# Kernel tuning notes

Hardware: AMD Instinct MI355X
Metric: run time of the kernel (lower is better)

Reference implementation:

```python
import jax, jax.numpy as jnp
import numpy as np

K = 5      # neighborhood size (k in torch module)
D_DIL = 4  # dilation (d in torch module)


def _neighbor_indices(H, W, k, d):
    # Matches torch: offsets = range(-(k//2)*d, k*(d//2)+1, d); pairs (i,j) added to (x,y), clamped.
    offs = np.arange(-(k // 2) * d, k * (d // 2) + 1, d)
    pairs = np.array([(i, j) for i in offs for j in offs])  # (k2, 2): i -> x offset, j -> y offset
    y, x = np.meshgrid(np.arange(H), np.arange(W), indexing='ij')
    xi = np.clip(x[None, :, :] + pairs[:, 0, None, None], 0, W - 1)  # (k2, H, W)
    yi = np.clip(y[None, :, :] + pairs[:, 1, None, None], 0, H - 1)  # (k2, H, W)
    return jnp.asarray(yi, jnp.int32), jnp.asarray(xi, jnp.int32)


def _safe_l2(diff):
    # L2 norm over last axis with a grad-safe zero (norm at 0 has subgradient 0, like torch).
    ss = jnp.sum(diff * diff, axis=-1)
    safe = jnp.where(ss > 0, ss, 1.0)
    return jnp.where(ss > 0, jnp.sqrt(safe), 0.0)


def setup_inputs() -> dict:
    key = jax.random.key(0)
    des = jax.random.normal(key, (2, 64, 384, 384), dtype=jnp.float32)
    return {"des": des}


def reference(des):
    B, D, H, W = des.shape
    k2 = K * K
    # per-pixel std of descriptor over channel dim
    mu = jnp.mean(des, axis=1)                                  # (B, H, W)
    s_abs = jnp.sqrt(jnp.mean(des * des, axis=1) - mu * mu)     # (B, H, W)

    des_p = jnp.transpose(des, (0, 2, 3, 1))                    # (B, H, W, D)
    yi, xi = _neighbor_indices(H, W, K, D_DIL)                  # (k2, H, W) each

    # Stream over k^2 neighbor offsets, accumulating L2 distances (avoids (B,k2,H,W,D) blowup).
    def body(acc, idx):
        y, x = idx
        nb = des_p[:, y, x, :]                                  # (B, H, W, D) gather
        return acc + _safe_l2(des_p - nb), None

    acc0 = jnp.zeros((B, H, W), des.dtype)
    acc, _ = jax.lax.scan(body, acc0, (yi, xi))
    s_rel = acc / k2                                            # (B, H, W)

    s_raw = s_abs * s_rel
    s = s_raw / (s_raw + 1.0)
    return s[:, None, :, :]                                     # (B, 1, H, W)
```

## Files before the change

### kernel.cpp

```cpp
#include <hip/hip_runtime.h>

#define HH 384
#define WW 384
#define HWP (HH * WW)
#define DD 64
#define BB 2
#define NG2 8

#define TX 16
#define TY 8
#define LR 24
#define LC 32
#define LN (LR * LC)
#define NT 64
#define SPT (LN / NT)
#define NBX (WW / TX)
#define NBY (HH / TY)
#define NWG (NBX * NBY * BB)

typedef __fp16 h2v __attribute__((ext_vector_type(2)));
union h4 { uint2 u; h2v h[2]; };

#if __has_builtin(__builtin_amdgcn_fdot2)
#define DOT4(acc, a, b)                                           \
    acc = __builtin_amdgcn_fdot2((a).h[0], (b).h[0], acc, false);   \
    acc = __builtin_amdgcn_fdot2((a).h[1], (b).h[1], acc, false)
#else
#define DOT4(acc, a, b)                                     \
    acc = fmaf((float)(a).h[0].x, (float)(b).h[0].x, acc);   \
    acc = fmaf((float)(a).h[0].y, (float)(b).h[0].y, acc);   \
    acc = fmaf((float)(a).h[1].x, (float)(b).h[1].x, acc);   \
    acc = fmaf((float)(a).h[1].y, (float)(b).h[1].y, acc)
#endif

__device__ __forceinline__ void gl_lds16(const uint4* g, uint4* l) {
    __builtin_amdgcn_global_load_lds(
        (const __attribute__((address_space(1))) unsigned int*)(const void*)g,
        (__attribute__((address_space(3))) unsigned int*)(void*)l, 16, 0, 0);
}

#define FENCE() asm volatile("" ::: "memory")

__global__ __launch_bounds__(256) void stats_pack_k(const float* __restrict__ des,
                                                    uint4* __restrict__ hp4,
                                                    float* __restrict__ ssq,
                                                    float* __restrict__ smm) {
    int idx = blockIdx.x * 256 + threadIdx.x;
    int b = idx / HWP;
    int p = idx - b * HWP;
    const float* base = des + (size_t)b * DD * HWP + p;
    uint4* hb = hp4 + (size_t)b * NG2 * HWP + p;
    float ss = 0.f, s0 = 0.f;
#pragma unroll 2
    for (int g = 0; g < NG2; ++g) {
        float v0 = base[(size_t)(8 * g + 0) * HWP];
        float v1 = base[(size_t)(8 * g + 1) * HWP];
        float v2 = base[(size_t)(8 * g + 2) * HWP];
        float v3 = base[(size_t)(8 * g + 3) * HWP];
        float v4 = base[(size_t)(8 * g + 4) * HWP];
        float v5 = base[(size_t)(8 * g + 5) * HWP];
        float v6 = base[(size_t)(8 * g + 6) * HWP];
        float v7 = base[(size_t)(8 * g + 7) * HWP];
        ss = fmaf(v0, v0, ss); ss = fmaf(v1, v1, ss);
        ss = fmaf(v2, v2, ss); ss = fmaf(v3, v3, ss);
        ss = fmaf(v4, v4, ss); ss = fmaf(v5, v5, ss);
        ss = fmaf(v6, v6, ss); ss = fmaf(v7, v7, ss);
        s0 += ((v0 + v1) + (v2 + v3)) + ((v4 + v5) + (v6 + v7));
        h4 a, c;
        a.h[0] = __builtin_amdgcn_cvt_pkrtz(v0, v1);
        a.h[1] = __builtin_amdgcn_cvt_pkrtz(v2, v3);
        c.h[0] = __builtin_amdgcn_cvt_pkrtz(v4, v5);
        c.h[1] = __builtin_amdgcn_cvt_pkrtz(v6, v7);
        uint4 w; w.x = a.u.x; w.y = a.u.y; w.z = c.u.x; w.w = c.u.y;
        hb[(size_t)g * HWP] = w;
    }
    ssq[idx] = ss;
    smm[idx] = s0;
}

__global__ __launch_bounds__(NT) void ssd_k(const uint4* __restrict__ hp4,
                                            const float* __restrict__ ssq,
                                            const float* __restrict__ smm,
                                            float* __restrict__ out) {
    __shared__ uint4 lds[2][LN];
    const int tid = threadIdx.x;
    const int tx = tid & 15;
    const int ty = tid >> 4;

    int bid = blockIdx.x;
    int swz = (bid & 7) * 288 + (bid >> 3);
    int b  = swz / (NBX * NBY);
    int r0 = swz % (NBX * NBY);
    int by = r0 / NBX;
    int bx = r0 - by * NBX;
    const int x0 = bx * TX, y0 = by * TY;
    const int x = x0 + tx;
    const int y = y0 + ty;

    int goff[SPT];
#pragma unroll
    for (int k = 0; k < SPT; ++k) {
        int i = tid + NT * k;
        int r = i / LC, c = i - (i / LC) * LC;
        int gy = y0 + r - 8; gy = gy < 0 ? 0 : (gy > HH - 1 ? HH - 1 : gy);
        int gx = x0 + c - 8; gx = gx < 0 ? 0 : (gx > WW - 1 ? WW - 1 : gx);
        goff[k] = gy * WW + gx;
    }

    const uint4* hb = hp4 + (size_t)b * NG2 * HWP;

    auto STAGE = [&](int g, int bb) {
        const uint4* p = hb + (size_t)g * HWP;
#pragma unroll
        for (int k = 0; k < SPT; ++k)
            gl_lds16(p + goff[k], &lds[bb][tid + NT * k]);
    };

    float accA[25], accB[25];
#pragma unroll
    for (int n = 0; n < 25; ++n) { accA[n] = 0.f; accB[n] = 0.f; }

    const int base = ty * LC + tx;
    auto COMPUTE = [&](int bb) {
        const uint4* L = lds[bb];
        uint4 cc0 = L[base + 8 * LC + 8];
        uint4 cc1 = L[base + 12 * LC + 8];
        h4 cA0, cA1, cB0, cB1;
        cA0.u.x = cc0.x; cA0.u.y = cc0.y; cA1.u.x = cc0.z; cA1.u.y = cc0.w;
        cB0.u.x = cc1.x; cB0.u.y = cc1.y; cB1.u.x = cc1.z; cB1.u.y = cc1.w;
#pragma unroll
        for (int m = 0; m < 6; ++m)
#pragma unroll
            for (int j = 0; j < 5; ++j) {
                uint4 v = L[base + (4 * m) * LC + 4 * j];
                h4 va, vb;
                va.u.x = v.x; va.u.y = v.y; vb.u.x = v.z; vb.u.y = v.w;
                if (m < 5) {
                    int n = m * 5 + j;
                    DOT4(accA[n], cA0, va);
                    DOT4(accA[n], cA1, vb);
                }
                if (m >= 1) {
                    int n = (m - 1) * 5 + j;
                    DOT4(accB[n], cB0, va);
                    DOT4(accB[n], cB1, vb);
                }
            }
    };

    STAGE(0, 0);
    STAGE(1, 1);
#pragma unroll 1
    for (int g = 0; g < NG2; ++g) {
        if (g < NG2 - 1) { asm volatile("s_waitcnt vmcnt(12)" ::: "memory"); }
        else             { asm volatile("s_waitcnt vmcnt(0)" ::: "memory"); }
        FENCE();
        COMPUTE(g & 1);
        FENCE();
        if (g + 2 < NG2) {
            asm volatile("s_waitcnt lgkmcnt(0)" ::: "memory");
            STAGE(g + 2, g & 1);
        }
    }

    asm volatile("s_waitcnt lgkmcnt(0)" ::: "memory");
    float* lsq = (float*)&lds[0][0];
    {
        const float* sp = ssq + (size_t)b * HWP;
        float r[SPT];
#pragma unroll
        for (int k = 0; k < SPT; ++k) r[k] = sp[goff[k]];
#pragma unroll
        for (int k = 0; k < SPT; ++k) lsq[tid + NT * k] = r[k];
    }
    FENCE();

    float sv[6][5];
#pragma unroll
    for (int m = 0; m < 6; ++m)
#pragma unroll
        for (int j = 0; j < 5; ++j)
            sv[m][j] = lsq[base + (4 * m) * LC + 4 * j];

    int yc[6], xc[5];
#pragma unroll
    for (int m = 0; m < 6; ++m) {
        int yy = y - 8 + 4 * m; yc[m] = yy < 0 ? 0 : (yy > HH - 1 ? HH - 1 : yy);
    }
#pragma unroll
    for (int j = 0; j < 5; ++j) {
        int xx = x - 8 + 4 * j; xc[j] = xx < 0 ? 0 : (xx > WW - 1 ? WW - 1 : xx);
    }

#pragma unroll
    for (int a = 0; a < 2; ++a) {
        const int py = y + 4 * a;
        const float* acc = a ? accB : accA;
        float ssA = sv[2 + a][2];
        float mu = smm[(size_t)b * HWP + py * WW + x] * (1.0f / 64);
        float var = ssA * (1.0f / 64) - mu * mu;
        float sabs = sqrtf(fmaxf(var, 0.f));
        float L = 0.f;
#pragma unroll
        for (int m = 0; m < 5; ++m)
#pragma unroll
            for (int j = 0; j < 5; ++j) {
                float ssB = sv[m + a][j];
                float d2 = fmaxf(ssA + ssB - 2.f * acc[m * 5 + j], 0.f);
                float sq = sqrtf(d2);
                L += (yc[m + a] == py && xc[j] == x) ? 0.f : sq;
            }
        float srel = L * (1.0f / 25);
        float sraw = sabs * srel;
        out[(size_t)b * HWP + py * WW + x] = sraw / (sraw + 1.f);
    }
}

extern "C" void kernel_launch(void* const* d_in, const int* in_sizes, int n_in,
                              void* d_out, int out_size, void* d_ws, size_t ws_size,
                              hipStream_t stream) {
    const float* des = (const float*)d_in[0];
    float* out = (float*)d_out;

    uint4* hp4 = (uint4*)d_ws;
    float* ssq = (float*)(hp4 + (size_t)BB * NG2 * HWP);
    float* smm = ssq + (size_t)BB * HWP;

    stats_pack_k<<<dim3((BB * HWP) / 256), dim3(256), 0, stream>>>(des, hp4, ssq, smm);
    ssd_k<<<dim3(NWG), dim3(NT), 0, stream>>>(hp4, ssq, smm, out);
}
```

Baseline: 48.50 us.

## Triple-buffer LDS staging, compute channel mean in fp16 dot, add setprio

Moves the LDS staging pipeline from double to triple buffering with adjusted vmcnt waits and a fully unrolled loop, so more global loads stay in flight. The per-pixel channel sum is dropped from the pack kernel and instead recomputed in the main kernel with fp16 dot products against ones, which removes one global write and one read. s_setprio is raised around the dot-product loop. The risks are higher LDS use (lower occupancy), and the mean now comes from fp16-rounded values, which slightly changes precision.

```diff
diff --git a/kernel.cpp b/kernel.cpp
--- a/kernel.cpp
+++ b/kernel.cpp
@@ -43,14 +43,13 @@
 
 __global__ __launch_bounds__(256) void stats_pack_k(const float* __restrict__ des,
                                                     uint4* __restrict__ hp4,
-                                                    float* __restrict__ ssq,
-                                                    float* __restrict__ smm) {
+                                                    float* __restrict__ ssq) {
     int idx = blockIdx.x * 256 + threadIdx.x;
     int b = idx / HWP;
     int p = idx - b * HWP;
     const float* base = des + (size_t)b * DD * HWP + p;
     uint4* hb = hp4 + (size_t)b * NG2 * HWP + p;
-    float ss = 0.f, s0 = 0.f;
+    float ss = 0.f;
 #pragma unroll 2
     for (int g = 0; g < NG2; ++g) {
         float v0 = base[(size_t)(8 * g + 0) * HWP];
@@ -65,7 +64,6 @@
         ss = fmaf(v2, v2, ss); ss = fmaf(v3, v3, ss);
         ss = fmaf(v4, v4, ss); ss = fmaf(v5, v5, ss);
         ss = fmaf(v6, v6, ss); ss = fmaf(v7, v7, ss);
-        s0 += ((v0 + v1) + (v2 + v3)) + ((v4 + v5) + (v6 + v7));
         h4 a, c;
         a.h[0] = __builtin_amdgcn_cvt_pkrtz(v0, v1);
         a.h[1] = __builtin_amdgcn_cvt_pkrtz(v2, v3);
@@ -75,14 +73,12 @@
         hb[(size_t)g * HWP] = w;
     }
     ssq[idx] = ss;
-    smm[idx] = s0;
 }
 
 __global__ __launch_bounds__(NT) void ssd_k(const uint4* __restrict__ hp4,
                                             const float* __restrict__ ssq,
-                                            const float* __restrict__ smm,
                                             float* __restrict__ out) {
-    __shared__ uint4 lds[2][LN];
+    __shared__ uint4 lds[3][LN];
     const int tid = threadIdx.x;
     const int tx = tid & 15;
     const int ty = tid >> 4;
@@ -119,6 +115,11 @@
     float accA[25], accB[25];
 #pragma unroll
     for (int n = 0; n < 25; ++n) { accA[n] = 0.f; accB[n] = 0.f; }
+    float smA = 0.f, smB = 0.f;
+
+    h4 ONE;
+    { h2v one2; one2.x = (__fp16)1.f; one2.y = (__fp16)1.f;
+      ONE.h[0] = one2; ONE.h[1] = one2; }
 
     const int base = ty * LC + tx;
     auto COMPUTE = [&](int bb) {
@@ -128,6 +129,9 @@
         h4 cA0, cA1, cB0, cB1;
         cA0.u.x = cc0.x; cA0.u.y = cc0.y; cA1.u.x = cc0.z; cA1.u.y = cc0.w;
         cB0.u.x = cc1.x; cB0.u.y = cc1.y; cB1.u.x = cc1.z; cB1.u.y = cc1.w;
+        DOT4(smA, cA0, ONE); DOT4(smA, cA1, ONE);
+        DOT4(smB, cB0, ONE); DOT4(smB, cB1, ONE);
+        __builtin_amdgcn_s_setprio(1);
 #pragma unroll
         for (int m = 0; m < 6; ++m)
 #pragma unroll
@@ -146,20 +150,23 @@
                     DOT4(accB[n], cB1, vb);
                 }
             }
+        __builtin_amdgcn_s_setprio(0);
     };
 
     STAGE(0, 0);
     STAGE(1, 1);
-#pragma unroll 1
+    STAGE(2, 2);
+#pragma unroll
     for (int g = 0; g < NG2; ++g) {
-        if (g < NG2 - 1) { asm volatile("s_waitcnt vmcnt(12)" ::: "memory"); }
-        else             { asm volatile("s_waitcnt vmcnt(0)" ::: "memory"); }
+        if (g < NG2 - 2)      { asm volatile("s_waitcnt vmcnt(24)" ::: "memory"); }
+        else if (g == NG2 - 2){ asm volatile("s_waitcnt vmcnt(12)" ::: "memory"); }
+        else                  { asm volatile("s_waitcnt vmcnt(0)"  ::: "memory"); }
         FENCE();
-        COMPUTE(g & 1);
+        COMPUTE(g % 3);
         FENCE();
-        if (g + 2 < NG2) {
+        if (g + 3 < NG2) {
             asm volatile("s_waitcnt lgkmcnt(0)" ::: "memory");
-            STAGE(g + 2, g & 1);
+            STAGE(g + 3, g % 3);
         }
     }
 
@@ -196,8 +203,9 @@
     for (int a = 0; a < 2; ++a) {
         const int py = y + 4 * a;
         const float* acc = a ? accB : accA;
+        float sm = a ? smB : smA;
         float ssA = sv[2 + a][2];
-        float mu = smm[(size_t)b * HWP + py * WW + x] * (1.0f / 64);
+        float mu = sm * (1.0f / 64);
         float var = ssA * (1.0f / 64) - mu * mu;
         float sabs = sqrtf(fmaxf(var, 0.f));
         float L = 0.f;
@@ -224,8 +232,7 @@
 
     uint4* hp4 = (uint4*)d_ws;
     float* ssq = (float*)(hp4 + (size_t)BB * NG2 * HWP);
-    float* smm = ssq + (size_t)BB * HWP;
-
-    stats_pack_k<<<dim3((BB * HWP) / 256), dim3(256), 0, stream>>>(des, hp4, ssq, smm);
-    ssd_k<<<dim3(NWG), dim3(NT), 0, stream>>>(hp4, ssq, smm, out);
-}
+
+    stats_pack_k<<<dim3((BB * HWP) / 256), dim3(256), 0, stream>>>(des, hp4, ssq);
+    ssd_k<<<dim3(NWG), dim3(NT), 0, stream>>>(hp4, ssq, out);
+}
```

Result: slower. 180.7 us (+272.6%).
